# Optimization experiments

Hardware: AMD Instinct MI355X
Metric: run time of the kernel (lower is better)

Reference implementation:

```python
import jax, jax.numpy as jnp
import numpy as np

B, C, H, W = 16, 192, 48, 48
EPS = 1e-5  # torch LayerNorm default


def setup_inputs() -> dict:
    key = jax.random.key(0)
    ks = jax.random.split(key, 5)
    dim = C
    x = jax.random.normal(ks[0], (B, C, H, W), dtype=jnp.float32)
    ln_w = jnp.ones((dim,), dtype=jnp.float32)
    ln_b = jnp.zeros((dim,), dtype=jnp.float32)
    s = 1.0 / np.sqrt(dim)
    Wq = jax.random.uniform(ks[1], (dim, dim), jnp.float32, -s, s)
    Wk = jax.random.uniform(ks[2], (dim, dim), jnp.float32, -s, s)
    Wv = jax.random.uniform(ks[3], (dim, dim), jnp.float32, -s, s)
    w1 = jnp.ones((1,), dtype=jnp.float32)
    w2 = jnp.ones((1,), dtype=jnp.float32)
    return {"x": x, "ln_w": ln_w, "ln_b": ln_b, "Wq": Wq, "Wk": Wk, "Wv": Wv, "w1": w1, "w2": w2}


def reference(x, ln_w, ln_b, Wq, Wk, Wv, w1, w2):
    b, c, h, w = x.shape
    # [B, C, H, W] -> [B, N, C]
    xf = x.reshape(b, c, h * w).transpose(0, 2, 1)
    # LayerNorm over channel dim
    mu = jnp.mean(xf, axis=-1, keepdims=True)
    var = jnp.mean(jnp.square(xf - mu), axis=-1, keepdims=True)
    xn = (xf - mu) * jax.lax.rsqrt(var + EPS) * ln_w + ln_b
    # torch Linear: y = x @ W^T
    Q = jnp.einsum('bnc,dc->bnd', xn, Wq)
    K = jnp.einsum('bnc,dc->bnd', xn, Wk)
    V = jnp.einsum('bnc,dc->bnd', xn, Wv)
    S = jnp.einsum('bnd,bmd->bnm', Q, K)  # [B, N, N]
    attn1 = jax.nn.softmax(S, axis=-1)
    attn2 = jnp.square(jax.nn.relu(S))
    # learned blend weights (softmax over two scalars)
    e1, e2 = jnp.exp(w1), jnp.exp(w2)
    denom = e1 + e2
    attn = (e1 / denom) * attn1 + (e2 / denom) * attn2
    out = jnp.einsum('bnm,bmd->bnd', attn, V)  # [B, N, C]
    out = out.transpose(0, 2, 1).reshape(b, c, h, w)
    return out + x
```

## Files before the change

### kernel.cpp

```cpp
#include <hip/hip_runtime.h>

#define NN 2304
#define CC 192
#define NBATCH 16

typedef unsigned short u16;
typedef __bf16 bf16x8 __attribute__((ext_vector_type(8)));
typedef float f32x4 __attribute__((ext_vector_type(4)));
typedef float f32x16 __attribute__((ext_vector_type(16)));

__device__ __forceinline__ u16 bf16bits(float f) {
  union { float f; unsigned u; } v;
  v.f = f;
  unsigned r = v.u + 0x7FFFu + ((v.u >> 16) & 1u);
  return (u16)(r >> 16);
}

__device__ __forceinline__ uint32_t cvtpk(float lo, float hi) {
  uint32_t d;
  asm("v_cvt_pk_bf16_f32 %0, %1, %2" : "=v"(d) : "v"(lo), "v"(hi));
  return d;
}

__device__ __forceinline__ int swzK(int row, int col) {
  int ch = col >> 3;
  int phys = (ch & ~7) | ((ch ^ row) & 7);
  return row * 192 + (phys << 3) + (col & 7);
}
__device__ __forceinline__ int swz64(int row, int col) {
  int ch = (col >> 3) ^ row;
  return (row << 6) | ((ch & 7) << 3) | (col & 7);
}

__device__ __forceinline__ void gll16(const u16* g, u16* l) {
  __builtin_amdgcn_global_load_lds(
      (const __attribute__((address_space(1))) u16*)g,
      (__attribute__((address_space(3))) u16*)l, 16, 0, 0);
}

__global__ __launch_bounds__(256) void ln_kernel(
    const float* __restrict__ x, const float* __restrict__ lnw,
    const float* __restrict__ lnb, u16* __restrict__ xn) {
  __shared__ float xt[192 * 65];
  __shared__ float psum[4][64], psq[4][64];
  __shared__ float mu_s[64], rs_s[64];
  __shared__ float lw_s[192], lb_s[192];
  int t = threadIdx.x;
  int b = blockIdx.y, n0 = blockIdx.x * 64;
  const float* xb = x + (size_t)b * CC * NN;
  if (t < 192) { lw_s[t] = lnw[t]; lb_s[t] = lnb[t]; }
#pragma unroll
  for (int i = 0; i < 48; ++i) {
    int idx = i * 256 + t;
    int c = idx >> 6, n = idx & 63;
    xt[c * 65 + n] = xb[(size_t)c * NN + n0 + n];
  }
  __syncthreads();
  {
    int n = t & 63, part = t >> 6;
    float s = 0.f, s2 = 0.f;
#pragma unroll
    for (int c = part * 48; c < part * 48 + 48; ++c) {
      float v = xt[c * 65 + n];
      s += v; s2 += v * v;
    }
    psum[part][n] = s; psq[part][n] = s2;
  }
  __syncthreads();
  if (t < 64) {
    float s = psum[0][t] + psum[1][t] + psum[2][t] + psum[3][t];
    float s2 = psq[0][t] + psq[1][t] + psq[2][t] + psq[3][t];
    float mu = s * (1.0f / 192.0f);
    float var = s2 * (1.0f / 192.0f) - mu * mu;
    mu_s[t] = mu;
    rs_s[t] = rsqrtf(var + 1e-5f);
  }
  __syncthreads();
#pragma unroll
  for (int i = 0; i < 12; ++i) {
    int u = i * 256 + t;
    int n = u / 48, cq = (u % 48) * 4;
    float mu = mu_s[n], rs = rs_s[n];
    float v0 = (xt[(cq + 0) * 65 + n] - mu) * rs * lw_s[cq + 0] + lb_s[cq + 0];
    float v1 = (xt[(cq + 1) * 65 + n] - mu) * rs * lw_s[cq + 1] + lb_s[cq + 1];
    float v2 = (xt[(cq + 2) * 65 + n] - mu) * rs * lw_s[cq + 2] + lb_s[cq + 2];
    float v3 = (xt[(cq + 3) * 65 + n] - mu) * rs * lw_s[cq + 3] + lb_s[cq + 3];
    uint2 o;
    o.x = cvtpk(v0, v1);
    o.y = cvtpk(v2, v3);
    *(uint2*)&xn[((size_t)(b * NN + n0 + n)) * CC + cq] = o;
  }
}

__global__ __launch_bounds__(256, 3) void qkv_gemm(
    const u16* __restrict__ xn, const float* __restrict__ Wq,
    const float* __restrict__ Wk, const float* __restrict__ Wv,
    u16* __restrict__ qb, u16* __restrict__ kb, u16* __restrict__ vtb) {
  __shared__ u16 xs[12288];
  __shared__ u16 wsm[12288];
  int t = threadIdx.x, w = t >> 6, lane = t & 63, l15 = lane & 15, qd = lane >> 4;
  int m0 = blockIdx.x * 64, n0 = blockIdx.y * 64, z = blockIdx.z;
  const float* W = (z == 0) ? Wq : (z == 1 ? Wk : Wv);
#pragma unroll
  for (int i = 0; i < 6; ++i) {
    int ch = i * 256 + t;
    int row = ch / 24, cin = (ch % 24) * 8;
    *(uint4*)&xs[swzK(row, cin)] = *(const uint4*)&xn[(size_t)(m0 + row) * 192 + cin];
  }
#pragma unroll
  for (int i = 0; i < 6; ++i) {
    int ch = i * 256 + t;
    int row = ch / 24, cin = (ch % 24) * 8;
    const float* src = &W[(size_t)(n0 + row) * 192 + cin];
    float4 f0 = *(const float4*)src;
    float4 f1 = *(const float4*)(src + 4);
    uint4 o;
    o.x = cvtpk(f0.x, f0.y);
    o.y = cvtpk(f0.z, f0.w);
    o.z = cvtpk(f1.x, f1.y);
    o.w = cvtpk(f1.z, f1.w);
    *(uint4*)&wsm[swzK(row, cin)] = o;
  }
  __syncthreads();
  bf16x8 a[6];
#pragma unroll
  for (int kk = 0; kk < 6; ++kk)
    a[kk] = *(const bf16x8*)&xs[swzK(w * 16 + l15, kk * 32 + qd * 8)];
  const f32x4 fz = {0.f, 0.f, 0.f, 0.f};
  f32x4 acc[4];
#pragma unroll
  for (int ct = 0; ct < 4; ++ct) {
    acc[ct] = fz;
#pragma unroll
    for (int kk = 0; kk < 6; ++kk) {
      bf16x8 bfr = *(const bf16x8*)&wsm[swzK(ct * 16 + l15, kk * 32 + qd * 8)];
      acc[ct] = __builtin_amdgcn_mfma_f32_16x16x32_bf16(a[kk], bfr, acc[ct], 0, 0, 0);
    }
  }
  if (z < 2) {
    u16* outp = (z == 0) ? qb : kb;
#pragma unroll
    for (int ct = 0; ct < 4; ++ct)
#pragma unroll
      for (int r = 0; r < 4; ++r) {
        int m = m0 + w * 16 + qd * 4 + r;
        outp[(size_t)m * 192 + n0 + ct * 16 + l15] = bf16bits(acc[ct][r]);
      }
  } else {
    __syncthreads();
#pragma unroll
    for (int ct = 0; ct < 4; ++ct)
#pragma unroll
      for (int r = 0; r < 4; ++r)
        xs[swz64(ct * 16 + l15, w * 16 + qd * 4 + r)] = bf16bits(acc[ct][r]);
    __syncthreads();
    int b = blockIdx.x / 36, nb = (blockIdx.x % 36) * 64;
#pragma unroll
    for (int i = 0; i < 16; ++i) {
      int idx = i * 256 + t;
      int d = idx >> 6, nn = idx & 63;
      vtb[(size_t)b * 192 * NN + (size_t)(n0 + d) * NN + nb + nn] = xs[swz64(d, nn)];
    }
  }
}

__global__ __launch_bounds__(256, 3) void attn_lsum(
    const u16* __restrict__ qb, const u16* __restrict__ kb,
    float* __restrict__ lsum_g) {
  __shared__ u16 sm[24576];
  __shared__ float lp[2][2][32];
  int t = threadIdx.x, w = t >> 6, lane = t & 63;
  int l31 = lane & 31, hi = lane >> 5;
  int qh = w >> 1, ch = w & 1;
  int bid = blockIdx.x;
  int xcd = bid & 7, j = bid >> 3;
  int b = xcd * 2 + (j >= 36 ? 1 : 0);
  int qt = (j >= 36) ? j - 36 : j;

  const u16* Kg = kb + (size_t)b * NN * CC;
  const u16* Qr = qb + ((size_t)b * NN + qt * 64 + qh * 32 + l31) * CC + hi * 8;
  bf16x8 qf[12];
#pragma unroll
  for (int ks = 0; ks < 12; ++ks) qf[ks] = *(const bf16x8*)(Qr + ks * 16);

#pragma unroll
  for (int i = 0; i < 6; ++i) {
    int cid = i * 4 + w, sc = cid * 64 + lane;
    int row = sc / 24, pc = sc % 24;
    int gc = (pc & ~7) | ((pc ^ row) & 7);
    gll16(Kg + (size_t)row * CC + gc * 8, sm + cid * 512);
  }

  f32x16 z16;
#pragma unroll
  for (int i = 0; i < 16; ++i) z16[i] = 0.f;
  float lsum = 0.f;

  for (int kt = 0; kt < 36; ++kt) {
    asm volatile("s_waitcnt vmcnt(0) lgkmcnt(0)\ns_barrier" ::: "memory");
    if (kt + 1 < 36) {
      u16* dst = sm + ((kt + 1) & 1) * 12288;
#pragma unroll
      for (int i = 0; i < 6; ++i) {
        int cid = i * 4 + w, sc = cid * 64 + lane;
        int row = sc / 24, pc = sc % 24;
        int gc = (pc & ~7) | ((pc ^ row) & 7);
        gll16(Kg + ((size_t)(kt + 1) * 64 + row) * CC + gc * 8, dst + cid * 512);
      }
    }
    const u16* kl = sm + (kt & 1) * 12288;
    f32x16 s0 = z16, s1 = z16;
    __builtin_amdgcn_s_setprio(1);
#pragma unroll
    for (int ks = 0; ks < 6; ++ks) {
      bf16x8 k0 = *(const bf16x8*)&kl[swzK(ch * 32 + l31, (2 * ks) * 16 + hi * 8)];
      bf16x8 k1 = *(const bf16x8*)&kl[swzK(ch * 32 + l31, (2 * ks + 1) * 16 + hi * 8)];
      s0 = __builtin_amdgcn_mfma_f32_32x32x16_bf16(k0, qf[2 * ks], s0, 0, 0, 0);
      s1 = __builtin_amdgcn_mfma_f32_32x32x16_bf16(k1, qf[2 * ks + 1], s1, 0, 0, 0);
    }
    __builtin_amdgcn_s_setprio(0);
#pragma unroll
    for (int r = 0; r < 16; ++r) {
      float s = s0[r] + s1[r];
      lsum += __expf(fminf(s, 60.f));
    }
  }
  lsum += __shfl_xor(lsum, 32);
  if (lane < 32) lp[qh][ch][l31] = lsum;
  __syncthreads();
  if (w == 0) {
    lsum_g[(size_t)b * NN + qt * 64 + lane] =
        lp[lane >> 5][0][lane & 31] + lp[lane >> 5][1][lane & 31];
  }
}

__global__ __launch_bounds__(256, 2) void attn_pv(
    const u16* __restrict__ qb, const u16* __restrict__ kb,
    const u16* __restrict__ vtb, const float* __restrict__ lsum_g,
    const float* __restrict__ w1p, const float* __restrict__ w2p,
    const float* __restrict__ x, float* __restrict__ out) {
  __shared__ u16 sm[28672];
  float* olds = (float*)sm;

  int t = threadIdx.x, w = t >> 6, lane = t & 63;
  int l31 = lane & 31, hi = lane >> 5;
  int qh = w >> 1, ch = w & 1;
  int bid = blockIdx.x;
  int xcd = bid & 7, j = bid >> 3;
  int b = xcd * 2 + (j >= 36 ? 1 : 0);
  int qt = (j >= 36) ? j - 36 : j;

  const u16* Kg = kb + (size_t)b * NN * CC;
  const u16* Vg = vtb + (size_t)b * CC * NN;
  const u16* Qr = qb + ((size_t)b * NN + qt * 64 + qh * 32 + l31) * CC + hi * 8;
  bf16x8 qf[12];
#pragma unroll
  for (int ks = 0; ks < 12; ++ks) qf[ks] = *(const bf16x8*)(Qr + ks * 16);

  float e1 = __expf(w1p[0]), e2 = __expf(w2p[0]);
  float den = e1 + e2;
  float c2f = e2 / den;
  float cl1 = (e1 / den) / lsum_g[(size_t)b * NN + qt * 64 + qh * 32 + l31];

  u16* pexW = sm + 24576 + (qh * 2 + ch) * 1024 + lane * 8;
  const u16* pexR = sm + 24576 + (qh * 2 + (1 - ch)) * 1024 + lane * 8;

  f32x16 z16;
#pragma unroll
  for (int i = 0; i < 16; ++i) z16[i] = 0.f;
  f32x16 os[3];
#pragma unroll
  for (int i = 0; i < 3; ++i) os[i] = z16;

#define STAGE_K(KT)                                                        \
  {                                                                        \
    _Pragma("unroll") for (int i = 0; i < 6; ++i) {                        \
      int cid = i * 4 + w, sc = cid * 64 + lane;                           \
      int row = sc / 24, pc = sc % 24;                                     \
      int gc = (pc & ~7) | ((pc ^ row) & 7);                               \
      gll16(Kg + ((size_t)(KT) * 64 + row) * CC + gc * 8, sm + cid * 512); \
    }                                                                      \
  }
#define STAGE_V(KT)                                                        \
  {                                                                        \
    _Pragma("unroll") for (int i = 0; i < 6; ++i) {                        \
      int cid = i * 4 + w, sc = cid * 64 + lane;                           \
      int d = sc >> 3, pc = sc & 7, gc = (pc ^ d) & 7;                     \
      gll16(Vg + (size_t)d * NN + (KT) * 64 + gc * 8,                      \
            sm + 12288 + cid * 512);                                       \
    }                                                                      \
  }

  alignas(16) uint32_t pOwn0[4], pOwn1[4];
#define S_BLEND()                                                           \
  {                                                                         \
    f32x16 sA0 = z16, sA1 = z16;                                            \
    __builtin_amdgcn_s_setprio(1);                                          \
    _Pragma("unroll") for (int ks = 0; ks < 6; ++ks) {                      \
      bf16x8 k0 =                                                           \
          *(const bf16x8*)&sm[swzK(ch * 32 + l31, (2 * ks) * 16 + hi * 8)]; \
      bf16x8 k1 =                                                           \
          *(const bf16x8*)&sm[swzK(ch * 32 + l31, (2 * ks + 1) * 16 + hi * 8)]; \
      sA0 = __builtin_amdgcn_mfma_f32_32x32x16_bf16(k0, qf[2 * ks], sA0, 0, 0, 0); \
      sA1 = __builtin_amdgcn_mfma_f32_32x32x16_bf16(k1, qf[2 * ks + 1], sA1, 0, 0, 0); \
    }                                                                       \
    __builtin_amdgcn_s_setprio(0);                                          \
    uint32_t W[8];                                                          \
    _Pragma("unroll") for (int g = 0; g < 4; ++g) {                         \
      float sv0 = sA0[4 * g + 0] + sA1[4 * g + 0];                          \
      float sv1 = sA0[4 * g + 1] + sA1[4 * g + 1];                          \
      float sv2 = sA0[4 * g + 2] + sA1[4 * g + 2];                          \
      float sv3 = sA0[4 * g + 3] + sA1[4 * g + 3];                          \
      float r0 = fmaxf(sv0, 0.f), r1 = fmaxf(sv1, 0.f);                     \
      float r2 = fmaxf(sv2, 0.f), r3 = fmaxf(sv3, 0.f);                     \
      float p0 = cl1 * __expf(fminf(sv0, 60.f)) + c2f * r0 * r0;            \
      float p1 = cl1 * __expf(fminf(sv1, 60.f)) + c2f * r1 * r1;            \
      float p2 = cl1 * __expf(fminf(sv2, 60.f)) + c2f * r2 * r2;            \
      float p3 = cl1 * __expf(fminf(sv3, 60.f)) + c2f * r3 * r3;            \
      W[2 * g] = cvtpk(p0, p1);                                             \
      W[2 * g + 1] = cvtpk(p2, p3);                                         \
    }                                                                       \
    uint32_t X[8];                                                          \
    _Pragma("unroll") for (int jj = 0; jj < 8; ++jj)                        \
        X[jj] = __shfl_xor(W[jj], 32);                                      \
    pOwn0[0] = hi ? X[2] : W[0]; pOwn0[1] = hi ? X[3] : W[1];               \
    pOwn0[2] = hi ? W[2] : X[0]; pOwn0[3] = hi ? W[3] : X[1];               \
    pOwn1[0] = hi ? X[6] : W[4]; pOwn1[1] = hi ? X[7] : W[5];               \
    pOwn1[2] = hi ? W[6] : X[4]; pOwn1[3] = hi ? W[7] : X[5];               \
    *(uint4*)pexW = *(uint4*)pOwn0;                                         \
    *(uint4*)(pexW + 512) = *(uint4*)pOwn1;                                 \
  }

  STAGE_K(0);
  STAGE_V(0);
  asm volatile("s_waitcnt vmcnt(6)\ns_barrier" ::: "memory");
  S_BLEND();
  asm volatile("s_waitcnt lgkmcnt(0)\ns_barrier" ::: "memory");
  STAGE_K(1);

  for (int kt = 0; kt < 36; ++kt) {
    if (kt == 35)
      asm volatile("s_waitcnt vmcnt(0) lgkmcnt(0)\ns_barrier" ::: "memory");
    else
      asm volatile("s_waitcnt vmcnt(6) lgkmcnt(0)\ns_barrier" ::: "memory");

    const u16* vl = sm + 12288;
    uint4 pb0 = *(const uint4*)pexR;
    uint4 pb1 = *(const uint4*)(pexR + 512);
    __builtin_amdgcn_s_setprio(1);
#pragma unroll
    for (int dt = 0; dt < 3; ++dt) {
      int d = ch * 96 + dt * 32 + l31;
      bf16x8 vo0 = *(const bf16x8*)&vl[swz64(d, (ch * 2 + 0) * 16 + hi * 8)];
      bf16x8 vo1 = *(const bf16x8*)&vl[swz64(d, (ch * 2 + 1) * 16 + hi * 8)];
      bf16x8 vs0 = *(const bf16x8*)&vl[swz64(d, ((1 - ch) * 2 + 0) * 16 + hi * 8)];
      bf16x8 vs1 = *(const bf16x8*)&vl[swz64(d, ((1 - ch) * 2 + 1) * 16 + hi * 8)];
      os[dt] = __builtin_amdgcn_mfma_f32_32x32x16_bf16(
          *(const bf16x8*)pOwn0, vo0, os[dt], 0, 0, 0);
      os[dt] = __builtin_amdgcn_mfma_f32_32x32x16_bf16(
          *(const bf16x8*)pOwn1, vo1, os[dt], 0, 0, 0);
      os[dt] = __builtin_amdgcn_mfma_f32_32x32x16_bf16(
          *(const bf16x8*)&pb0, vs0, os[dt], 0, 0, 0);
      os[dt] = __builtin_amdgcn_mfma_f32_32x32x16_bf16(
          *(const bf16x8*)&pb1, vs1, os[dt], 0, 0, 0);
    }
    __builtin_amdgcn_s_setprio(0);

    if (kt < 35) {
      asm volatile("s_waitcnt vmcnt(0) lgkmcnt(0)\ns_barrier" ::: "memory");
      STAGE_V(kt + 1);
      S_BLEND();
      asm volatile("s_waitcnt lgkmcnt(0)\ns_barrier" ::: "memory");
      if (kt + 2 < 36) STAGE_K(kt + 2);
    }
  }

  __syncthreads();
#pragma unroll
  for (int dt = 0; dt < 3; ++dt) {
    int d = ch * 96 + dt * 32 + l31;
#pragma unroll
    for (int r = 0; r < 16; ++r) {
      int m = (r & 3) + 8 * (r >> 2) + 4 * hi;
      int q = qh * 32 + m;
      olds[d * 64 + ((q & ~31) | ((q ^ d) & 31))] = os[dt][r];
    }
  }
  __syncthreads();
  const float* xb = x + (size_t)b * CC * NN + qt * 64;
  float* ob = out + (size_t)b * CC * NN + qt * 64;
#pragma unroll
  for (int i = 0; i < 48; ++i) {
    int idx = i * 256 + t;
    int c = idx >> 6, nn = idx & 63;
    float v = olds[c * 64 + ((nn & ~31) | ((nn ^ c) & 31))];
    ob[(size_t)c * NN + nn] = v + xb[(size_t)c * NN + nn];
  }
#undef STAGE_K
#undef STAGE_V
#undef S_BLEND
}

extern "C" void kernel_launch(void* const* d_in, const int* in_sizes, int n_in,
                              void* d_out, int out_size, void* d_ws, size_t ws_size,
                              hipStream_t stream) {
  (void)in_sizes; (void)n_in; (void)out_size; (void)ws_size;
  const float* x   = (const float*)d_in[0];
  const float* lnw = (const float*)d_in[1];
  const float* lnb = (const float*)d_in[2];
  const float* Wq  = (const float*)d_in[3];
  const float* Wk  = (const float*)d_in[4];
  const float* Wv  = (const float*)d_in[5];
  const float* w1  = (const float*)d_in[6];
  const float* w2  = (const float*)d_in[7];
  float* out = (float*)d_out;

  u16* xn = (u16*)d_ws;
  size_t per = (size_t)NBATCH * NN * CC;
  u16* qb  = xn + per;
  u16* kb  = qb + per;
  u16* vtb = kb + per;
  float* lsum_g = (float*)d_ws;

  ln_kernel<<<dim3(36, 16), 256, 0, stream>>>(x, lnw, lnb, xn);
  qkv_gemm<<<dim3(576, 3, 3), 256, 0, stream>>>(xn, Wq, Wk, Wv, qb, kb, vtb);
  attn_lsum<<<dim3(576), 256, 0, stream>>>(qb, kb, lsum_g);
  attn_pv<<<dim3(576), 256, 0, stream>>>(qb, kb, vtb, lsum_g, w1, w2, x, out);
}
```

Before: 295.3 us.

## Fuse softmax row-sum pass into PV kernel with split softmax/relu² accumulators

Removes the separate QK^T pass that computed softmax denominators. Unnormalized exp and relu² weights now go into two separate PV accumulators, and the exp row-sum is reduced at the end to apply the normalization. This avoids recomputing QK^T, re-reading K, and one kernel launch. In exchange it doubles the PV MFMA work, adds 48 accumulator registers, and doubles the LDS exchange traffic per tile.

```diff
diff --git a/kernel.cpp b/kernel.cpp
--- a/kernel.cpp
+++ b/kernel.cpp
@@ -164,11 +164,15 @@
   }
 }
 
-__global__ __launch_bounds__(256, 3) void attn_lsum(
+__global__ __launch_bounds__(256, 2) void attn_fused(
     const u16* __restrict__ qb, const u16* __restrict__ kb,
-    float* __restrict__ lsum_g) {
-  __shared__ u16 sm[24576];
-  __shared__ float lp[2][2][32];
+    const u16* __restrict__ vtb, const float* __restrict__ w1p,
+    const float* __restrict__ w2p, const float* __restrict__ x,
+    float* __restrict__ out) {
+  __shared__ u16 sm[32768];
+  float* olds = (float*)sm;
+  float* lred = (float*)(sm + 24576);
+
   int t = threadIdx.x, w = t >> 6, lane = t & 63;
   int l31 = lane & 31, hi = lane >> 5;
   int qh = w >> 1, ch = w & 1;
@@ -178,79 +182,6 @@
   int qt = (j >= 36) ? j - 36 : j;
 
   const u16* Kg = kb + (size_t)b * NN * CC;
-  const u16* Qr = qb + ((size_t)b * NN + qt * 64 + qh * 32 + l31) * CC + hi * 8;
-  bf16x8 qf[12];
-#pragma unroll
-  for (int ks = 0; ks < 12; ++ks) qf[ks] = *(const bf16x8*)(Qr + ks * 16);
-
-#pragma unroll
-  for (int i = 0; i < 6; ++i) {
-    int cid = i * 4 + w, sc = cid * 64 + lane;
-    int row = sc / 24, pc = sc % 24;
-    int gc = (pc & ~7) | ((pc ^ row) & 7);
-    gll16(Kg + (size_t)row * CC + gc * 8, sm + cid * 512);
-  }
-
-  f32x16 z16;
-#pragma unroll
-  for (int i = 0; i < 16; ++i) z16[i] = 0.f;
-  float lsum = 0.f;
-
-  for (int kt = 0; kt < 36; ++kt) {
-    asm volatile("s_waitcnt vmcnt(0) lgkmcnt(0)\ns_barrier" ::: "memory");
-    if (kt + 1 < 36) {
-      u16* dst = sm + ((kt + 1) & 1) * 12288;
-#pragma unroll
-      for (int i = 0; i < 6; ++i) {
-        int cid = i * 4 + w, sc = cid * 64 + lane;
-        int row = sc / 24, pc = sc % 24;
-        int gc = (pc & ~7) | ((pc ^ row) & 7);
-        gll16(Kg + ((size_t)(kt + 1) * 64 + row) * CC + gc * 8, dst + cid * 512);
-      }
-    }
-    const u16* kl = sm + (kt & 1) * 12288;
-    f32x16 s0 = z16, s1 = z16;
-    __builtin_amdgcn_s_setprio(1);
-#pragma unroll
-    for (int ks = 0; ks < 6; ++ks) {
-      bf16x8 k0 = *(const bf16x8*)&kl[swzK(ch * 32 + l31, (2 * ks) * 16 + hi * 8)];
-      bf16x8 k1 = *(const bf16x8*)&kl[swzK(ch * 32 + l31, (2 * ks + 1) * 16 + hi * 8)];
-      s0 = __builtin_amdgcn_mfma_f32_32x32x16_bf16(k0, qf[2 * ks], s0, 0, 0, 0);
-      s1 = __builtin_amdgcn_mfma_f32_32x32x16_bf16(k1, qf[2 * ks + 1], s1, 0, 0, 0);
-    }
-    __builtin_amdgcn_s_setprio(0);
-#pragma unroll
-    for (int r = 0; r < 16; ++r) {
-      float s = s0[r] + s1[r];
-      lsum += __expf(fminf(s, 60.f));
-    }
-  }
-  lsum += __shfl_xor(lsum, 32);
-  if (lane < 32) lp[qh][ch][l31] = lsum;
-  __syncthreads();
-  if (w == 0) {
-    lsum_g[(size_t)b * NN + qt * 64 + lane] =
-        lp[lane >> 5][0][lane & 31] + lp[lane >> 5][1][lane & 31];
-  }
-}
-
-__global__ __launch_bounds__(256, 2) void attn_pv(
-    const u16* __restrict__ qb, const u16* __restrict__ kb,
-    const u16* __restrict__ vtb, const float* __restrict__ lsum_g,
-    const float* __restrict__ w1p, const float* __restrict__ w2p,
-    const float* __restrict__ x, float* __restrict__ out) {
-  __shared__ u16 sm[28672];
-  float* olds = (float*)sm;
-
-  int t = threadIdx.x, w = t >> 6, lane = t & 63;
-  int l31 = lane & 31, hi = lane >> 5;
-  int qh = w >> 1, ch = w & 1;
-  int bid = blockIdx.x;
-  int xcd = bid & 7, j = bid >> 3;
-  int b = xcd * 2 + (j >= 36 ? 1 : 0);
-  int qt = (j >= 36) ? j - 36 : j;
-
-  const u16* Kg = kb + (size_t)b * NN * CC;
   const u16* Vg = vtb + (size_t)b * CC * NN;
   const u16* Qr = qb + ((size_t)b * NN + qt * 64 + qh * 32 + l31) * CC + hi * 8;
   bf16x8 qf[12];
@@ -259,18 +190,20 @@
 
   float e1 = __expf(w1p[0]), e2 = __expf(w2p[0]);
   float den = e1 + e2;
-  float c2f = e2 / den;
-  float cl1 = (e1 / den) / lsum_g[(size_t)b * NN + qt * 64 + qh * 32 + l31];
-
-  u16* pexW = sm + 24576 + (qh * 2 + ch) * 1024 + lane * 8;
-  const u16* pexR = sm + 24576 + (qh * 2 + (1 - ch)) * 1024 + lane * 8;
+  float c1f = e1 / den, c2f = e2 / den;
+
+  u16* pexSW = sm + 24576 + (qh * 2 + ch) * 1024 + lane * 8;
+  const u16* pexSR = sm + 24576 + (qh * 2 + (1 - ch)) * 1024 + lane * 8;
+  u16* pexRW = sm + 28672 + (qh * 2 + ch) * 1024 + lane * 8;
+  const u16* pexRR = sm + 28672 + (qh * 2 + (1 - ch)) * 1024 + lane * 8;
 
   f32x16 z16;
 #pragma unroll
   for (int i = 0; i < 16; ++i) z16[i] = 0.f;
-  f32x16 os[3];
-#pragma unroll
-  for (int i = 0; i < 3; ++i) os[i] = z16;
+  f32x16 os[3], orl[3];
+#pragma unroll
+  for (int i = 0; i < 3; ++i) { os[i] = z16; orl[i] = z16; }
+  float lsum = 0.f;
 
 #define STAGE_K(KT)                                                        \
   {                                                                        \
@@ -291,7 +224,7 @@
     }                                                                      \
   }
 
-  alignas(16) uint32_t pOwn0[4], pOwn1[4];
+  alignas(16) uint32_t pS0[4], pS1[4], pR0[4], pR1[4];
 #define S_BLEND()                                                           \
   {                                                                         \
     f32x16 sA0 = z16, sA1 = z16;                                            \
@@ -305,30 +238,41 @@
       sA1 = __builtin_amdgcn_mfma_f32_32x32x16_bf16(k1, qf[2 * ks + 1], sA1, 0, 0, 0); \
     }                                                                       \
     __builtin_amdgcn_s_setprio(0);                                          \
-    uint32_t W[8];                                                          \
+    uint32_t WS[8], WR[8];                                                  \
     _Pragma("unroll") for (int g = 0; g < 4; ++g) {                         \
       float sv0 = sA0[4 * g + 0] + sA1[4 * g + 0];                          \
       float sv1 = sA0[4 * g + 1] + sA1[4 * g + 1];                          \
       float sv2 = sA0[4 * g + 2] + sA1[4 * g + 2];                          \
       float sv3 = sA0[4 * g + 3] + sA1[4 * g + 3];                          \
+      float e0 = __expf(fminf(sv0, 60.f));                                  \
+      float e1v = __expf(fminf(sv1, 60.f));                                 \
+      float e2v = __expf(fminf(sv2, 60.f));                                 \
+      float e3 = __expf(fminf(sv3, 60.f));                                  \
       float r0 = fmaxf(sv0, 0.f), r1 = fmaxf(sv1, 0.f);                     \
       float r2 = fmaxf(sv2, 0.f), r3 = fmaxf(sv3, 0.f);                     \
-      float p0 = cl1 * __expf(fminf(sv0, 60.f)) + c2f * r0 * r0;            \
-      float p1 = cl1 * __expf(fminf(sv1, 60.f)) + c2f * r1 * r1;            \
-      float p2 = cl1 * __expf(fminf(sv2, 60.f)) + c2f * r2 * r2;            \
-      float p3 = cl1 * __expf(fminf(sv3, 60.f)) + c2f * r3 * r3;            \
-      W[2 * g] = cvtpk(p0, p1);                                             \
-      W[2 * g + 1] = cvtpk(p2, p3);                                         \
+      lsum += (e0 + e1v) + (e2v + e3);                                      \
+      WS[2 * g] = cvtpk(e0, e1v);                                           \
+      WS[2 * g + 1] = cvtpk(e2v, e3);                                       \
+      WR[2 * g] = cvtpk(r0 * r0, r1 * r1);                                  \
+      WR[2 * g + 1] = cvtpk(r2 * r2, r3 * r3);                              \
     }                                                                       \
-    uint32_t X[8];                                                          \
-    _Pragma("unroll") for (int jj = 0; jj < 8; ++jj)                        \
-        X[jj] = __shfl_xor(W[jj], 32);                                      \
-    pOwn0[0] = hi ? X[2] : W[0]; pOwn0[1] = hi ? X[3] : W[1];               \
-    pOwn0[2] = hi ? W[2] : X[0]; pOwn0[3] = hi ? W[3] : X[1];               \
-    pOwn1[0] = hi ? X[6] : W[4]; pOwn1[1] = hi ? X[7] : W[5];               \
-    pOwn1[2] = hi ? W[6] : X[4]; pOwn1[3] = hi ? W[7] : X[5];               \
-    *(uint4*)pexW = *(uint4*)pOwn0;                                         \
-    *(uint4*)(pexW + 512) = *(uint4*)pOwn1;                                 \
+    uint32_t XS[8], XR[8];                                                  \
+    _Pragma("unroll") for (int jj = 0; jj < 8; ++jj) {                      \
+      XS[jj] = __shfl_xor(WS[jj], 32);                                      \
+      XR[jj] = __shfl_xor(WR[jj], 32);                                      \
+    }                                                                       \
+    pS0[0] = hi ? XS[2] : WS[0]; pS0[1] = hi ? XS[3] : WS[1];               \
+    pS0[2] = hi ? WS[2] : XS[0]; pS0[3] = hi ? WS[3] : XS[1];               \
+    pS1[0] = hi ? XS[6] : WS[4]; pS1[1] = hi ? XS[7] : WS[5];               \
+    pS1[2] = hi ? WS[6] : XS[4]; pS1[3] = hi ? WS[7] : XS[5];               \
+    pR0[0] = hi ? XR[2] : WR[0]; pR0[1] = hi ? XR[3] : WR[1];               \
+    pR0[2] = hi ? WR[2] : XR[0]; pR0[3] = hi ? WR[3] : XR[1];               \
+    pR1[0] = hi ? XR[6] : WR[4]; pR1[1] = hi ? XR[7] : WR[5];               \
+    pR1[2] = hi ? WR[6] : XR[4]; pR1[3] = hi ? WR[7] : XR[5];               \
+    *(uint4*)pexSW = *(uint4*)pS0;                                          \
+    *(uint4*)(pexSW + 512) = *(uint4*)pS1;                                  \
+    *(uint4*)pexRW = *(uint4*)pR0;                                          \
+    *(uint4*)(pexRW + 512) = *(uint4*)pR1;                                  \
   }
 
   STAGE_K(0);
@@ -345,8 +289,10 @@
       asm volatile("s_waitcnt vmcnt(6) lgkmcnt(0)\ns_barrier" ::: "memory");
 
     const u16* vl = sm + 12288;
-    uint4 pb0 = *(const uint4*)pexR;
-    uint4 pb1 = *(const uint4*)(pexR + 512);
+    uint4 sS0 = *(const uint4*)pexSR;
+    uint4 sS1 = *(const uint4*)(pexSR + 512);
+    uint4 sR0 = *(const uint4*)pexRR;
+    uint4 sR1 = *(const uint4*)(pexRR + 512);
     __builtin_amdgcn_s_setprio(1);
 #pragma unroll
     for (int dt = 0; dt < 3; ++dt) {
@@ -356,13 +302,21 @@
       bf16x8 vs0 = *(const bf16x8*)&vl[swz64(d, ((1 - ch) * 2 + 0) * 16 + hi * 8)];
       bf16x8 vs1 = *(const bf16x8*)&vl[swz64(d, ((1 - ch) * 2 + 1) * 16 + hi * 8)];
       os[dt] = __builtin_amdgcn_mfma_f32_32x32x16_bf16(
-          *(const bf16x8*)pOwn0, vo0, os[dt], 0, 0, 0);
+          *(const bf16x8*)pS0, vo0, os[dt], 0, 0, 0);
+      orl[dt] = __builtin_amdgcn_mfma_f32_32x32x16_bf16(
+          *(const bf16x8*)pR0, vo0, orl[dt], 0, 0, 0);
       os[dt] = __builtin_amdgcn_mfma_f32_32x32x16_bf16(
-          *(const bf16x8*)pOwn1, vo1, os[dt], 0, 0, 0);
+          *(const bf16x8*)pS1, vo1, os[dt], 0, 0, 0);
+      orl[dt] = __builtin_amdgcn_mfma_f32_32x32x16_bf16(
+          *(const bf16x8*)pR1, vo1, orl[dt], 0, 0, 0);
       os[dt] = __builtin_amdgcn_mfma_f32_32x32x16_bf16(
-          *(const bf16x8*)&pb0, vs0, os[dt], 0, 0, 0);
+          *(const bf16x8*)&sS0, vs0, os[dt], 0, 0, 0);
+      orl[dt] = __builtin_amdgcn_mfma_f32_32x32x16_bf16(
+          *(const bf16x8*)&sR0, vs0, orl[dt], 0, 0, 0);
       os[dt] = __builtin_amdgcn_mfma_f32_32x32x16_bf16(
-          *(const bf16x8*)&pb1, vs1, os[dt], 0, 0, 0);
+          *(const bf16x8*)&sS1, vs1, os[dt], 0, 0, 0);
+      orl[dt] = __builtin_amdgcn_mfma_f32_32x32x16_bf16(
+          *(const bf16x8*)&sR1, vs1, orl[dt], 0, 0, 0);
     }
     __builtin_amdgcn_s_setprio(0);
 
@@ -375,6 +329,17 @@
     }
   }
 
+  lsum += __shfl_xor(lsum, 32);
+  __syncthreads();
+  if (lane < 32) lred[(qh * 2 + ch) * 32 + l31] = lsum;
+  __syncthreads();
+  float linv[16];
+#pragma unroll
+  for (int r = 0; r < 16; ++r) {
+    int m = (r & 3) + 8 * (r >> 2) + 4 * hi;
+    float ltot = lred[(qh * 2 + 0) * 32 + m] + lred[(qh * 2 + 1) * 32 + m];
+    linv[r] = c1f / ltot;
+  }
   __syncthreads();
 #pragma unroll
   for (int dt = 0; dt < 3; ++dt) {
@@ -383,7 +348,8 @@
     for (int r = 0; r < 16; ++r) {
       int m = (r & 3) + 8 * (r >> 2) + 4 * hi;
       int q = qh * 32 + m;
-      olds[d * 64 + ((q & ~31) | ((q ^ d) & 31))] = os[dt][r];
+      olds[d * 64 + ((q & ~31) | ((q ^ d) & 31))] =
+          os[dt][r] * linv[r] + c2f * orl[dt][r];
     }
   }
   __syncthreads();
@@ -420,10 +386,8 @@
   u16* qb  = xn + per;
   u16* kb  = qb + per;
   u16* vtb = kb + per;
-  float* lsum_g = (float*)d_ws;
 
   ln_kernel<<<dim3(36, 16), 256, 0, stream>>>(x, lnw, lnb, xn);
   qkv_gemm<<<dim3(576, 3, 3), 256, 0, stream>>>(xn, Wq, Wk, Wv, qb, kb, vtb);
-  attn_lsum<<<dim3(576), 256, 0, stream>>>(qb, kb, lsum_g);
-  attn_pv<<<dim3(576), 256, 0, stream>>>(qb, kb, vtb, lsum_g, w1, w2, x, out);
-}
+  attn_fused<<<dim3(576), 256, 0, stream>>>(qb, kb, vtb, w1, w2, x, out);
+}
```

Result: faster. 283.1 us (-4.1%).

## Prebake bf16 weights, reuse xn tile across Q/K/V, async LDS loads

Applied to the files above, without the earlier changes.

Adds a small kernel that converts Wq/Wk/Wv to bf16 once, so the QKV GEMM no longer converts fp32 weights per block. Each GEMM block now loops over the three projections, loading the xn tile once and prefetching the next weight tile with direct global-to-LDS loads while it writes the current outputs. It also raises attn_pv's occupancy hint from 2 to 3 blocks per SM. The risks are register pressure in attn_pv from the tighter launch bound and one extra kernel launch.

```diff
diff --git a/kernel.cpp b/kernel.cpp
--- a/kernel.cpp
+++ b/kernel.cpp
@@ -92,74 +92,97 @@
   }
 }
 
+__global__ __launch_bounds__(256) void wconv_kernel(
+    const float* __restrict__ Wq, const float* __restrict__ Wk,
+    const float* __restrict__ Wv, u16* __restrict__ wbf) {
+  int z = blockIdx.y;
+  const float* W = (z == 0) ? Wq : (z == 1 ? Wk : Wv);
+  u16* o = wbf + (size_t)z * 36864;
+  int idx = (blockIdx.x * 256 + (int)threadIdx.x) * 8;
+  float4 f0 = *(const float4*)&W[idx];
+  float4 f1 = *(const float4*)&W[idx + 4];
+  uint4 v;
+  v.x = cvtpk(f0.x, f0.y);
+  v.y = cvtpk(f0.z, f0.w);
+  v.z = cvtpk(f1.x, f1.y);
+  v.w = cvtpk(f1.z, f1.w);
+  *(uint4*)&o[idx] = v;
+}
+
 __global__ __launch_bounds__(256, 3) void qkv_gemm(
-    const u16* __restrict__ xn, const float* __restrict__ Wq,
-    const float* __restrict__ Wk, const float* __restrict__ Wv,
+    const u16* __restrict__ xn, const u16* __restrict__ wbf,
     u16* __restrict__ qb, u16* __restrict__ kb, u16* __restrict__ vtb) {
   __shared__ u16 xs[12288];
   __shared__ u16 wsm[12288];
   int t = threadIdx.x, w = t >> 6, lane = t & 63, l15 = lane & 15, qd = lane >> 4;
-  int m0 = blockIdx.x * 64, n0 = blockIdx.y * 64, z = blockIdx.z;
-  const float* W = (z == 0) ? Wq : (z == 1 ? Wk : Wv);
+  int m0 = blockIdx.x * 64, n0 = blockIdx.y * 64;
+
 #pragma unroll
   for (int i = 0; i < 6; ++i) {
-    int ch = i * 256 + t;
-    int row = ch / 24, cin = (ch % 24) * 8;
-    *(uint4*)&xs[swzK(row, cin)] = *(const uint4*)&xn[(size_t)(m0 + row) * 192 + cin];
+    int cid = i * 4 + w, sc = cid * 64 + lane;
+    int row = sc / 24, pc = sc % 24;
+    int gc = (pc & ~7) | ((pc ^ row) & 7);
+    gll16(xn + (size_t)(m0 + row) * 192 + gc * 8, xs + cid * 512);
   }
 #pragma unroll
   for (int i = 0; i < 6; ++i) {
-    int ch = i * 256 + t;
-    int row = ch / 24, cin = (ch % 24) * 8;
-    const float* src = &W[(size_t)(n0 + row) * 192 + cin];
-    float4 f0 = *(const float4*)src;
-    float4 f1 = *(const float4*)(src + 4);
-    uint4 o;
-    o.x = cvtpk(f0.x, f0.y);
-    o.y = cvtpk(f0.z, f0.w);
-    o.z = cvtpk(f1.x, f1.y);
-    o.w = cvtpk(f1.z, f1.w);
-    *(uint4*)&wsm[swzK(row, cin)] = o;
-  }
-  __syncthreads();
+    int cid = i * 4 + w, sc = cid * 64 + lane;
+    int row = sc / 24, pc = sc % 24;
+    int gc = (pc & ~7) | ((pc ^ row) & 7);
+    gll16(wbf + (size_t)(n0 + row) * 192 + gc * 8, wsm + cid * 512);
+  }
+
   bf16x8 a[6];
-#pragma unroll
-  for (int kk = 0; kk < 6; ++kk)
-    a[kk] = *(const bf16x8*)&xs[swzK(w * 16 + l15, kk * 32 + qd * 8)];
   const f32x4 fz = {0.f, 0.f, 0.f, 0.f};
-  f32x4 acc[4];
-#pragma unroll
-  for (int ct = 0; ct < 4; ++ct) {
-    acc[ct] = fz;
-#pragma unroll
-    for (int kk = 0; kk < 6; ++kk) {
-      bf16x8 bfr = *(const bf16x8*)&wsm[swzK(ct * 16 + l15, kk * 32 + qd * 8)];
-      acc[ct] = __builtin_amdgcn_mfma_f32_16x16x32_bf16(a[kk], bfr, acc[ct], 0, 0, 0);
-    }
-  }
-  if (z < 2) {
-    u16* outp = (z == 0) ? qb : kb;
-#pragma unroll
-    for (int ct = 0; ct < 4; ++ct)
-#pragma unroll
-      for (int r = 0; r < 4; ++r) {
-        int m = m0 + w * 16 + qd * 4 + r;
-        outp[(size_t)m * 192 + n0 + ct * 16 + l15] = bf16bits(acc[ct][r]);
+  for (int z = 0; z < 3; ++z) {
+    asm volatile("s_waitcnt vmcnt(0) lgkmcnt(0)\ns_barrier" ::: "memory");
+    if (z == 0) {
+#pragma unroll
+      for (int kk = 0; kk < 6; ++kk)
+        a[kk] = *(const bf16x8*)&xs[swzK(w * 16 + l15, kk * 32 + qd * 8)];
+    }
+    f32x4 acc[4];
+#pragma unroll
+    for (int ct = 0; ct < 4; ++ct) {
+      acc[ct] = fz;
+#pragma unroll
+      for (int kk = 0; kk < 6; ++kk) {
+        bf16x8 bfr = *(const bf16x8*)&wsm[swzK(ct * 16 + l15, kk * 32 + qd * 8)];
+        acc[ct] = __builtin_amdgcn_mfma_f32_16x16x32_bf16(a[kk], bfr, acc[ct], 0, 0, 0);
       }
-  } else {
-    __syncthreads();
-#pragma unroll
-    for (int ct = 0; ct < 4; ++ct)
-#pragma unroll
-      for (int r = 0; r < 4; ++r)
-        xs[swz64(ct * 16 + l15, w * 16 + qd * 4 + r)] = bf16bits(acc[ct][r]);
-    __syncthreads();
-    int b = blockIdx.x / 36, nb = (blockIdx.x % 36) * 64;
-#pragma unroll
-    for (int i = 0; i < 16; ++i) {
-      int idx = i * 256 + t;
-      int d = idx >> 6, nn = idx & 63;
-      vtb[(size_t)b * 192 * NN + (size_t)(n0 + d) * NN + nb + nn] = xs[swz64(d, nn)];
+    }
+    asm volatile("s_waitcnt lgkmcnt(0)\ns_barrier" ::: "memory");
+    if (z < 2) {
+#pragma unroll
+      for (int i = 0; i < 6; ++i) {
+        int cid = i * 4 + w, sc = cid * 64 + lane;
+        int row = sc / 24, pc = sc % 24;
+        int gc = (pc & ~7) | ((pc ^ row) & 7);
+        gll16(wbf + (size_t)(z + 1) * 36864 + (size_t)(n0 + row) * 192 + gc * 8,
+              wsm + cid * 512);
+      }
+      u16* outp = (z == 0) ? qb : kb;
+#pragma unroll
+      for (int ct = 0; ct < 4; ++ct)
+#pragma unroll
+        for (int r = 0; r < 4; ++r) {
+          int m = m0 + w * 16 + qd * 4 + r;
+          outp[(size_t)m * 192 + n0 + ct * 16 + l15] = bf16bits(acc[ct][r]);
+        }
+    } else {
+#pragma unroll
+      for (int ct = 0; ct < 4; ++ct)
+#pragma unroll
+        for (int r = 0; r < 4; ++r)
+          xs[swz64(ct * 16 + l15, w * 16 + qd * 4 + r)] = bf16bits(acc[ct][r]);
+      __syncthreads();
+      int bb = blockIdx.x / 36, nb = (blockIdx.x % 36) * 64;
+#pragma unroll
+      for (int i = 0; i < 16; ++i) {
+        int idx = i * 256 + t;
+        int d = idx >> 6, nn = idx & 63;
+        vtb[(size_t)bb * 192 * NN + (size_t)(n0 + d) * NN + nb + nn] = xs[swz64(d, nn)];
+      }
     }
   }
 }
@@ -234,7 +257,7 @@
   }
 }
 
-__global__ __launch_bounds__(256, 2) void attn_pv(
+__global__ __launch_bounds__(256, 3) void attn_pv(
     const u16* __restrict__ qb, const u16* __restrict__ kb,
     const u16* __restrict__ vtb, const float* __restrict__ lsum_g,
     const float* __restrict__ w1p, const float* __restrict__ w2p,
@@ -420,10 +443,12 @@
   u16* qb  = xn + per;
   u16* kb  = qb + per;
   u16* vtb = kb + per;
+  u16* wbf = vtb + per;
   float* lsum_g = (float*)d_ws;
 
   ln_kernel<<<dim3(36, 16), 256, 0, stream>>>(x, lnw, lnb, xn);
-  qkv_gemm<<<dim3(576, 3, 3), 256, 0, stream>>>(xn, Wq, Wk, Wv, qb, kb, vtb);
+  wconv_kernel<<<dim3(18, 3), 256, 0, stream>>>(Wq, Wk, Wv, wbf);
+  qkv_gemm<<<dim3(576, 3), 256, 0, stream>>>(xn, wbf, qb, kb, vtb);
   attn_lsum<<<dim3(576), 256, 0, stream>>>(qb, kb, lsum_g);
   attn_pv<<<dim3(576), 256, 0, stream>>>(qb, kb, vtb, lsum_g, w1, w2, x, out);
 }
```

Result: no change. 295.8 us (+0.2%).
